# Optimization experiments

Measured on AMD Instinct MI355X. Metric: run time of the kernel, lower is better.

Reference implementation:

```python
import jax, jax.numpy as jnp
import numpy as np

B, C, F, NH, DK, DV = 16, 256, 32, 8, 32, 64
S = F * F
EPS = 1e-5
SCALE = DK ** -0.5


def _bn(t, g, b, m, v):
    # t: [B, Ch, H, W]; eval-mode batchnorm with running stats
    inv = g / jnp.sqrt(v + EPS)
    return t * inv[None, :, None, None] + (b - m * inv)[None, :, None, None]


def setup_inputs() -> dict:
    key = jax.random.key(0)
    ks = jax.random.split(key, 24)
    n = lambda i, shape, s=0.05: jax.random.normal(ks[i], shape, jnp.float32) * s
    u = lambda i, shape: jax.random.uniform(ks[i], shape, jnp.float32, 0.5, 1.5)
    # relative-position index table (buffer)
    r = np.arange(F)
    pos = np.stack(np.meshgrid(r, r, indexing='ij'), axis=-1).reshape(-1, 2)
    rel = np.abs(pos[:, None, :] - pos[None, :, :])
    pos_indices = jnp.asarray(rel[..., 0] * F + rel[..., 1], jnp.int32)  # [S, S]
    return {
        'x': jax.random.normal(ks[0], (B, C, F, F), jnp.float32),
        'Wq': n(1, (NH * DK, C)), 'q_g': u(2, (NH * DK,)), 'q_b': n(3, (NH * DK,)), 'q_m': n(4, (NH * DK,)), 'q_v': u(5, (NH * DK,)),
        'Wk': n(6, (NH * DK, C)), 'k_g': u(7, (NH * DK,)), 'k_b': n(8, (NH * DK,)), 'k_m': n(9, (NH * DK,)), 'k_v': u(10, (NH * DK,)),
        'Wv': n(11, (NH * DV, C)), 'v_g': u(12, (NH * DV,)), 'v_b': n(13, (NH * DV,)), 'v_m': n(14, (NH * DV,)), 'v_v': u(15, (NH * DV,)),
        'pos_emb': n(16, (F * F, NH)),
        'Wo': n(17, (C, NH * DV)), 'bo': n(18, (C,)),
        'o_g': u(19, (C,)), 'o_b': n(20, (C,)), 'o_m': n(21, (C,)), 'o_v': u(22, (C,)),
        'pos_indices': pos_indices,
    }


def reference(x, Wq, q_g, q_b, q_m, q_v, Wk, k_g, k_b, k_m, k_v, Wv, v_g, v_b, v_m, v_v,
              pos_emb, Wo, bo, o_g, o_b, o_m, o_v, pos_indices):
    # 1x1 conv == channel GEMM
    q = _bn(jnp.einsum('bchw,oc->bohw', x, Wq), q_g, q_b, q_m, q_v)
    k = _bn(jnp.einsum('bchw,oc->bohw', x, Wk), k_g, k_b, k_m, k_v)
    v = _bn(jnp.einsum('bchw,oc->bohw', x, Wv), v_g, v_b, v_m, v_v)
    # b (n d) h w -> b n s d
    qh = q.reshape(B, NH, DK, S).transpose(0, 1, 3, 2)
    kh = k.reshape(B, NH, DK, S).transpose(0, 1, 3, 2)
    vh = v.reshape(B, NH, DV, S).transpose(0, 1, 3, 2)
    attn = jnp.einsum('bnqd,bnkd->bnqk', qh, kh) * SCALE  # [B, NH, S, S]
    bias = pos_emb[pos_indices]                            # [S, S, NH] gather
    attn = attn + jnp.transpose(bias, (2, 0, 1))[None] / SCALE
    attn = jax.nn.softmax(attn, axis=-1)
    o = jnp.einsum('bnqk,bnkd->bnqd', attn, vh)            # [B, NH, S, DV]
    o = o.transpose(0, 1, 3, 2).reshape(B, NH * DV, F, F)  # b (n d) h w
    o = jax.nn.gelu(o, approximate=False)                  # torch default GELU (erf)
    o = jnp.einsum('bchw,oc->bohw', o, Wo) + bo[None, :, None, None]
    return _bn(o, o_g, o_b, o_m, o_v)
```

## Files before the change

kernel.cpp:

```cpp
#include <hip/hip_runtime.h>

#define B_ 16
#define C_ 256
#define NH_ 8
#define DK_ 32
#define DV_ 64
#define S_ 1024
#define CV_ 512

typedef __bf16 bf16;
typedef bf16 bf16x4 __attribute__((ext_vector_type(4)));
typedef bf16 bf16x8 __attribute__((ext_vector_type(8)));
typedef float f32x4 __attribute__((ext_vector_type(4)));

constexpr float EPSV = 1e-5f;
constexpr float SCALE_ = 0.17677669529663687f;
constexpr float LOG2E_ = 1.4426950408889634f;
constexpr float QSCALE_ = SCALE_ * LOG2E_;
constexpr float BSCALE_ = (1.0f / SCALE_) * LOG2E_;

__global__ void prep_kernel(const float* __restrict__ Wq, const float* __restrict__ qg, const float* __restrict__ qb, const float* __restrict__ qm, const float* __restrict__ qv,
                            const float* __restrict__ Wk, const float* __restrict__ kg, const float* __restrict__ kb, const float* __restrict__ km, const float* __restrict__ kv,
                            const float* __restrict__ Wv, const float* __restrict__ vg, const float* __restrict__ vb, const float* __restrict__ vm, const float* __restrict__ vv,
                            const float* __restrict__ Wo, const float* __restrict__ bo, const float* __restrict__ og_, const float* __restrict__ ob_, const float* __restrict__ om_, const float* __restrict__ ov_,
                            bf16* __restrict__ wqkv, float* __restrict__ bqkv, bf16* __restrict__ wo2, float* __restrict__ bo2) {
  int idx = blockIdx.x * 256 + threadIdx.x;
  if (idx < 1024 * 256) {
    int o = idx >> 8, c = idx & 255;
    float w, g, v;
    if (o < 256)      { w = Wq[o * 256 + c];        g = qg[o];       v = qv[o]; }
    else if (o < 512) { w = Wk[(o - 256) * 256 + c]; g = kg[o - 256]; v = kv[o - 256]; }
    else              { w = Wv[(o - 512) * 256 + c]; g = vg[o - 512]; v = vv[o - 512]; }
    float inv = g * rsqrtf(v + EPSV);
    wqkv[idx] = (bf16)(w * inv);
    if (c == 0) {
      float bb, m;
      if (o < 256)      { bb = qb[o];       m = qm[o]; }
      else if (o < 512) { bb = kb[o - 256]; m = km[o - 256]; }
      else              { bb = vb[o - 512]; m = vm[o - 512]; }
      bqkv[o] = bb - m * inv;
    }
  } else {
    int j = idx - 1024 * 256;
    if (j < 256 * 512) {
      int co = j >> 9, cv = j & 511;
      float inv = og_[co] * rsqrtf(ov_[co] + EPSV);
      wo2[j] = (bf16)(Wo[j] * inv);
      if (cv == 0) bo2[co] = bo[co] * inv + ob_[co] - om_[co] * inv;
    }
  }
}

__global__ __launch_bounds__(256) void xpose_kernel(const float* __restrict__ x, bf16* __restrict__ xT) {
  __shared__ bf16 t[64][66];
  int b = blockIdx.z, c0 = blockIdx.y * 64, s0 = blockIdx.x * 64;
  const float* xp = x + ((size_t)b * C_ + c0) * S_ + s0;
#pragma unroll
  for (int p = 0; p < 4; ++p) {
    int q = p * 256 + threadIdx.x;
    int ci = q >> 4, si4 = (q & 15) * 4;
    float4 v = *(const float4*)(xp + (size_t)ci * S_ + si4);
    t[si4 + 0][ci] = (bf16)v.x;
    t[si4 + 1][ci] = (bf16)v.y;
    t[si4 + 2][ci] = (bf16)v.z;
    t[si4 + 3][ci] = (bf16)v.w;
  }
  __syncthreads();
  bf16* op = xT + ((size_t)b * S_ + s0) * C_ + c0;
#pragma unroll
  for (int p = 0; p < 4; ++p) {
    int q = p * 256 + threadIdx.x;
    int si = q >> 4, ci4 = (q & 15) * 4;
    bf16x4 pk;
#pragma unroll
    for (int e = 0; e < 4; ++e) pk[e] = t[si][ci4 + e];
    *(bf16x4*)(op + (size_t)si * C_ + ci4) = pk;
  }
}

__device__ __forceinline__ void gload16(const void* g, void* l) {
  __builtin_amdgcn_global_load_lds((const __attribute__((address_space(1))) void*)g,
                                   (__attribute__((address_space(3))) void*)l, 16, 0, 0);
}

__global__ __launch_bounds__(256) void qkv_gemm_kernel(const bf16* __restrict__ wqkv, const float* __restrict__ bqkv,
                                                       const bf16* __restrict__ xT, bf16* __restrict__ qh,
                                                       bf16* __restrict__ kh, bf16* __restrict__ vT) {
  __shared__ bf16 alds[2][128 * 32];
  __shared__ bf16 blds[2][128 * 32];
  const int b = blockIdx.z;
  const int ob = blockIdx.y * 128, sb = blockIdx.x * 128;
  const int w = threadIdx.x >> 6, lane = threadIdx.x & 63;
  const int g = lane >> 4, lo = lane & 15;
  const int ow = (w >> 1) * 64, sw = (w & 1) * 64;

  const int r0 = threadIdx.x >> 2, c4 = threadIdx.x & 3;
  const int swz = (c4 ^ ((r0 >> 1) & 3)) * 8;
  const bf16* aS = wqkv + (size_t)(ob + r0) * C_ + swz;
  const bf16* bS = xT + ((size_t)b * S_ + sb + r0) * C_ + swz;
  const int ldst = threadIdx.x * 8;
  auto stage = [&](int buf, int kc) {
    gload16(aS + kc, &alds[buf][ldst]);
    gload16(aS + (size_t)64 * C_ + kc, &alds[buf][ldst + 2048]);
    gload16(bS + kc, &blds[buf][ldst]);
    gload16(bS + (size_t)64 * C_ + kc, &blds[buf][ldst + 2048]);
  };

  f32x4 acc[4][4] = {};

  stage(0, 0);
  __syncthreads();

  for (int step = 0; step < 8; ++step) {
    const int cur = step & 1;
    if (step < 7) stage(cur ^ 1, (step + 1) * 32);
    bf16x8 af[4], bfr[4];
    const int ch = (g ^ ((lo >> 1) & 3)) * 8;
#pragma unroll
    for (int i = 0; i < 4; ++i)
      af[i] = *(const bf16x8*)(&alds[cur][(ow + i * 16 + lo) * 32 + ch]);
#pragma unroll
    for (int j = 0; j < 4; ++j)
      bfr[j] = *(const bf16x8*)(&blds[cur][(sw + j * 16 + lo) * 32 + ch]);
#pragma unroll
    for (int i = 0; i < 4; ++i)
#pragma unroll
      for (int j = 0; j < 4; ++j)
        acc[i][j] = __builtin_amdgcn_mfma_f32_16x16x32_bf16(af[i], bfr[j], acc[i][j], 0, 0, 0);
    __syncthreads();
  }

#pragma unroll
  for (int i = 0; i < 4; ++i) {
    const int o0 = ob + ow + i * 16 + 4 * g;
    const bool isv = o0 >= 512;
    const bool isq = o0 < 256;
    float bias4[4];
#pragma unroll
    for (int r = 0; r < 4; ++r) bias4[r] = bqkv[o0 + r];
#pragma unroll
    for (int j = 0; j < 4; ++j) {
      const int s = sb + sw + j * 16 + lo;
      if (!isv) {
        const int n = (o0 >> 5) & 7;
        const int d0 = o0 & 31;
        bf16x4 pk;
#pragma unroll
        for (int r = 0; r < 4; ++r) {
          float v = acc[i][j][r] + bias4[r];
          pk[r] = (bf16)(isq ? v * QSCALE_ : v);
        }
        bf16* dst = (isq ? qh : kh) + (((size_t)b * NH_ + n) * S_ + s) * DK_ + d0;
        *(bf16x4*)dst = pk;
      } else {
        const int o2 = o0 - 512;
        const int n = o2 >> 6, dv0 = o2 & 63;
#pragma unroll
        for (int r = 0; r < 4; ++r)
          vT[(((size_t)b * NH_ + n) * DV_ + dv0 + r) * S_ + s] = (bf16)(acc[i][j][r] + bias4[r]);
      }
    }
  }
}

__global__ __launch_bounds__(512, 4) void attn_kernel(const bf16* __restrict__ qh, const bf16* __restrict__ kh,
                                                      const bf16* __restrict__ vT, const float* __restrict__ pos_emb,
                                                      bf16* __restrict__ og) {
  __shared__ f32x4 E4[32][64];
  __shared__ bf16 klds[2][64 * 32];
  __shared__ bf16 vlds[2][64 * 64];
  const int n = blockIdx.x, qt = blockIdx.y, b = blockIdx.z;
  const int w = threadIdx.x >> 6, lane = threadIdx.x & 63;
  const int g = lane >> 4, lo = lane & 15;
  const size_t bn = (size_t)b * NH_ + n;
  const bf16* __restrict__ kbase = kh + bn * (size_t)S_ * DK_;
  const bf16* __restrict__ vbase = vT + bn * (size_t)DV_ * S_;

  const int krow = (w & 3) * 16 + (lane >> 2), kslot = lane & 3;
  const int vrow = w * 8 + (lane >> 3), vslot = lane & 7;
  const bf16* ksrc0 = kbase + (size_t)krow * DK_ + ((kslot ^ ((krow >> 2) & 3)) * 8);
  const bf16* vsrc0 = vbase + (size_t)vrow * S_ + ((vslot ^ (vrow & 7)) * 8);
  auto stage = [&](int buf, int kt) {
    if (w < 4) gload16(ksrc0 + (size_t)kt * DK_, &klds[buf][(w & 3) * 512]);
    gload16(vsrc0 + kt, &vlds[buf][w * 512]);
  };

  stage(0, 0);

  for (int i = threadIdx.x; i < 32 * 64; i += 512) {
    const int dr = i >> 6, d = i & 63;
    f32x4 v;
#pragma unroll
    for (int j = 0; j < 4; ++j) {
      int dc = d - 28 - j;
      dc = dc < 0 ? -dc : dc;
      dc = dc > 31 ? 31 : dc;
      v[j] = pos_emb[(dr * 32 + dc) * NH_ + n] * BSCALE_;
    }
    E4[dr][d] = v;
  }

  const int qbase = qt * 256 + w * 32;
  const int q0 = qbase + lo, q1 = qbase + 16 + lo;
  const bf16x8 qf0 = *(const bf16x8*)(qh + (bn * S_ + q0) * DK_ + 8 * g);
  const bf16x8 qf1 = *(const bf16x8*)(qh + (bn * S_ + q1) * DK_ + 8 * g);
  const int qr = qbase >> 5;
  const int i00m = 12 + lo - 4 * g;

  f32x4 acc[4][2] = {};
  f32x4 lac[2] = {};
  bf16x8 ones;
#pragma unroll
  for (int j = 0; j < 8; ++j) ones[j] = (bf16)1.0f;

  asm volatile("s_waitcnt vmcnt(0)" ::: "memory");
  __syncthreads();

  const f32x4* __restrict__ E4f = &E4[0][0];

  for (int it = 0; it < 16; ++it) {
    const int kt = it * 64;
    const int cur = it & 1;
    if (it < 15) stage(cur ^ 1, kt + 64);
    const bf16* kbuf = &klds[cur][0];
    const bf16* vbuf = &vlds[cur][0];

    int dq = qr - 2 * it;
    int dra = dq < 0 ? -dq : dq;
    int dqb = dq - 1;
    int drb = dqb < 0 ? -dqb : dqb;
    const f32x4* pa = E4f + dra * 64 + i00m;
    const f32x4* pbq = E4f + drb * 64 + i00m;
    const f32x4 W0a = pa[16], W0b = pbq[16];

    bf16x8 pb[2][2];
#pragma unroll
    for (int u = 0; u < 4; ++u) {
      const int row = u * 16 + lo;
      bf16x8 ka = *(const bf16x8*)(kbuf + row * 32 + ((8 * g) ^ (((row >> 2) & 3) << 3)));
      f32x4 c0, c1;
      if (u == 0)      { c0 = W0a;    c1 = pa[32]; }
      else if (u == 1) { c0 = pa[0];  c1 = W0a; }
      else if (u == 2) { c0 = W0b;    c1 = pbq[32]; }
      else             { c0 = pbq[0]; c1 = W0b; }
      f32x4 s0 = __builtin_amdgcn_mfma_f32_16x16x32_bf16(ka, qf0, c0, 0, 0, 0);
      f32x4 s1 = __builtin_amdgcn_mfma_f32_16x16x32_bf16(ka, qf1, c1, 0, 0, 0);
      const int cb = (u & 1) * 4;
      const int up = u >> 1;
#pragma unroll
      for (int r = 0; r < 4; ++r) {
        pb[0][up][cb + r] = (bf16)__builtin_amdgcn_exp2f(s0[r]);
        pb[1][up][cb + r] = (bf16)__builtin_amdgcn_exp2f(s1[r]);
      }
    }

    __builtin_amdgcn_s_setprio(1);
    lac[0] = __builtin_amdgcn_mfma_f32_16x16x32_bf16(ones, pb[0][0], lac[0], 0, 0, 0);
    lac[0] = __builtin_amdgcn_mfma_f32_16x16x32_bf16(ones, pb[0][1], lac[0], 0, 0, 0);
    lac[1] = __builtin_amdgcn_mfma_f32_16x16x32_bf16(ones, pb[1][0], lac[1], 0, 0, 0);
    lac[1] = __builtin_amdgcn_mfma_f32_16x16x32_bf16(ones, pb[1][1], lac[1], 0, 0, 0);

#pragma unroll
    for (int t = 0; t < 4; ++t) {
      const int row = t * 16 + lo;
      const int rsw = row & 7;
      const bf16* vrow_p = vbuf + row * 64 + 4 * (g & 1);
      const int ghalf = g >> 1;
#pragma unroll
      for (int up = 0; up < 2; ++up) {
        bf16x4 a0 = *(const bf16x4*)(vrow_p + ((((4 * up + 0) + ghalf) ^ rsw) << 3));
        bf16x4 a1 = *(const bf16x4*)(vrow_p + ((((4 * up + 2) + ghalf) ^ rsw) << 3));
        bf16x8 va = __builtin_shufflevector(a0, a1, 0, 1, 2, 3, 4, 5, 6, 7);
        acc[t][0] = __builtin_amdgcn_mfma_f32_16x16x32_bf16(va, pb[0][up], acc[t][0], 0, 0, 0);
        acc[t][1] = __builtin_amdgcn_mfma_f32_16x16x32_bf16(va, pb[1][up], acc[t][1], 0, 0, 0);
      }
    }
    __builtin_amdgcn_s_setprio(0);

    asm volatile("s_waitcnt vmcnt(0)" ::: "memory");
    __syncthreads();
  }

#pragma unroll
  for (int h = 0; h < 2; ++h) {
    const float rinv = __builtin_amdgcn_rcpf(lac[h][0]);
    const int qx = qbase + 16 * h + lo;
    bf16* op = og + ((size_t)b * S_ + qx) * CV_ + n * DV_;
#pragma unroll
    for (int t = 0; t < 4; ++t) {
      bf16x4 pk;
#pragma unroll
      for (int r = 0; r < 4; ++r) {
        float xo = acc[t][h][r] * rinv;
        pk[r] = (bf16)(0.5f * xo * (1.f + erff(xo * 0.70710678118654752f)));
      }
      *(bf16x4*)(op + t * 16 + 4 * g) = pk;
    }
  }
}

__global__ __launch_bounds__(256) void out_gemm_kernel(const bf16* __restrict__ wo2, const float* __restrict__ bo2,
                                                       const bf16* __restrict__ og, float* __restrict__ out) {
  __shared__ bf16 alds[2][64 * 32];
  __shared__ bf16 blds[2][128 * 32];
  const int b = blockIdx.z;
  const int cb = blockIdx.y * 64, sb = blockIdx.x * 128;
  const int w = threadIdx.x >> 6, lane = threadIdx.x & 63;
  const int g = lane >> 4, lo = lane & 15;
  const int cw = (w >> 1) * 32, sw = (w & 1) * 64;

  const int r0 = threadIdx.x >> 2, c4 = threadIdx.x & 3;
  const int swz = (c4 ^ ((r0 >> 1) & 3)) * 8;
  const bf16* aS = wo2 + (size_t)(cb + r0) * CV_ + swz;
  const bf16* bS = og + ((size_t)b * S_ + sb + r0) * CV_ + swz;
  const int ldst = threadIdx.x * 8;
  auto stage = [&](int buf, int kc) {
    gload16(aS + kc, &alds[buf][ldst]);
    gload16(bS + kc, &blds[buf][ldst]);
    gload16(bS + (size_t)64 * CV_ + kc, &blds[buf][ldst + 2048]);
  };

  f32x4 acc[2][4] = {};

  stage(0, 0);
  __syncthreads();

  for (int step = 0; step < 16; ++step) {
    const int cur = step & 1;
    if (step < 15) stage(cur ^ 1, (step + 1) * 32);
    bf16x8 af[2], bfr[4];
    const int ch = (g ^ ((lo >> 1) & 3)) * 8;
#pragma unroll
    for (int i = 0; i < 2; ++i)
      af[i] = *(const bf16x8*)(&alds[cur][(cw + i * 16 + lo) * 32 + ch]);
#pragma unroll
    for (int j = 0; j < 4; ++j)
      bfr[j] = *(const bf16x8*)(&blds[cur][(sw + j * 16 + lo) * 32 + ch]);
#pragma unroll
    for (int i = 0; i < 2; ++i)
#pragma unroll
      for (int j = 0; j < 4; ++j)
        acc[i][j] = __builtin_amdgcn_mfma_f32_16x16x32_bf16(af[i], bfr[j], acc[i][j], 0, 0, 0);
    __syncthreads();
  }

#pragma unroll
  for (int i = 0; i < 2; ++i) {
    const int c0 = cb + cw + i * 16 + 4 * g;
    float bias4[4];
#pragma unroll
    for (int r = 0; r < 4; ++r) bias4[r] = bo2[c0 + r];
#pragma unroll
    for (int j = 0; j < 4; ++j) {
      const int s = sb + sw + j * 16 + lo;
#pragma unroll
      for (int r = 0; r < 4; ++r)
        out[((size_t)b * C_ + c0 + r) * S_ + s] = acc[i][j][r] + bias4[r];
    }
  }
}

extern "C" void kernel_launch(void* const* d_in, const int* in_sizes, int n_in,
                              void* d_out, int out_size, void* d_ws, size_t ws_size,
                              hipStream_t stream) {
  (void)in_sizes; (void)n_in; (void)out_size; (void)ws_size;
  const float* x   = (const float*)d_in[0];
  const float* Wq  = (const float*)d_in[1];
  const float* qg  = (const float*)d_in[2];
  const float* qb  = (const float*)d_in[3];
  const float* qm  = (const float*)d_in[4];
  const float* qv  = (const float*)d_in[5];
  const float* Wk  = (const float*)d_in[6];
  const float* kg  = (const float*)d_in[7];
  const float* kb  = (const float*)d_in[8];
  const float* km  = (const float*)d_in[9];
  const float* kv  = (const float*)d_in[10];
  const float* Wv  = (const float*)d_in[11];
  const float* vg  = (const float*)d_in[12];
  const float* vb  = (const float*)d_in[13];
  const float* vm  = (const float*)d_in[14];
  const float* vv  = (const float*)d_in[15];
  const float* pos = (const float*)d_in[16];
  const float* Wo  = (const float*)d_in[17];
  const float* bo  = (const float*)d_in[18];
  const float* ogm = (const float*)d_in[19];
  const float* obt = (const float*)d_in[20];
  const float* omn = (const float*)d_in[21];
  const float* ovr = (const float*)d_in[22];
  float* out = (float*)d_out;

  char* ws = (char*)d_ws;
  size_t off = 0;
  auto take = [&](size_t bytes) { char* p = ws + off; off += (bytes + 255) & ~(size_t)255; return p; };
  bf16*  wqkv = (bf16*) take((size_t)1024 * 256 * 2);
  float* bqkv = (float*)take(1024 * 4);
  bf16*  wo2  = (bf16*) take((size_t)256 * 512 * 2);
  float* bo2  = (float*)take(256 * 4);
  bf16*  xT   = (bf16*) take((size_t)B_ * S_ * C_ * 2);
  bf16*  qhb  = (bf16*) take((size_t)B_ * NH_ * S_ * DK_ * 2);
  bf16*  khb  = (bf16*) take((size_t)B_ * NH_ * S_ * DK_ * 2);
  bf16*  vTb  = (bf16*) take((size_t)B_ * NH_ * DV_ * S_ * 2);
  bf16*  ogb  = (bf16*) take((size_t)B_ * S_ * CV_ * 2);

  prep_kernel<<<dim3(1536), dim3(256), 0, stream>>>(Wq, qg, qb, qm, qv, Wk, kg, kb, km, kv,
                                                    Wv, vg, vb, vm, vv, Wo, bo, ogm, obt, omn, ovr,
                                                    wqkv, bqkv, wo2, bo2);
  xpose_kernel<<<dim3(16, 4, 16), dim3(256), 0, stream>>>(x, xT);
  qkv_gemm_kernel<<<dim3(8, 8, 16), dim3(256), 0, stream>>>(wqkv, bqkv, xT, qhb, khb, vTb);
  attn_kernel<<<dim3(8, 4, 16), dim3(512), 0, stream>>>(qhb, khb, vTb, pos, ogb);
  out_gemm_kernel<<<dim3(8, 4, 16), dim3(256), 0, stream>>>(wo2, bo2, ogb, out);
}
```

Baseline: 90.38 us.

## Split attention key range across two wave groups with LDS reduction, bf16 bias table

Each attention block now covers 128 queries instead of 256, and its two halves of 4 waves each process separate halves of the key sequence in 32-key tiles. Partial outputs and row sums are combined through LDS before the GELU epilogue. The block count doubles and launch bounds are raised, aiming at more parallelism and occupancy. The position-bias table is stored in bf16 to cut LDS use, which loses some precision in the bias and in the bf16-rounded partial outputs.

```diff
diff --git a/kernel.cpp b/kernel.cpp
--- a/kernel.cpp
+++ b/kernel.cpp
@@ -163,49 +163,53 @@
   }
 }
 
-__global__ __launch_bounds__(512, 4) void attn_kernel(const bf16* __restrict__ qh, const bf16* __restrict__ kh,
+__global__ __launch_bounds__(512, 8) void attn_kernel(const bf16* __restrict__ qh, const bf16* __restrict__ kh,
                                                       const bf16* __restrict__ vT, const float* __restrict__ pos_emb,
                                                       bf16* __restrict__ og) {
-  __shared__ f32x4 E4[32][64];
-  __shared__ bf16 klds[2][64 * 32];
-  __shared__ bf16 vlds[2][64 * 64];
+  __shared__ __align__(16) char smem[40960];
+  bf16* E4b = (bf16*)smem;
+  bf16* kld = (bf16*)(smem + 16384);
+  bf16* vld = (bf16*)(smem + 24576);
   const int n = blockIdx.x, qt = blockIdx.y, b = blockIdx.z;
   const int w = threadIdx.x >> 6, lane = threadIdx.x & 63;
   const int g = lane >> 4, lo = lane & 15;
+  const int h2 = w >> 2, wg = w & 3;
   const size_t bn = (size_t)b * NH_ + n;
   const bf16* __restrict__ kbase = kh + bn * (size_t)S_ * DK_;
   const bf16* __restrict__ vbase = vT + bn * (size_t)DV_ * S_;
-
-  const int krow = (w & 3) * 16 + (lane >> 2), kslot = lane & 3;
-  const int vrow = w * 8 + (lane >> 3), vslot = lane & 7;
-  const bf16* ksrc0 = kbase + (size_t)krow * DK_ + ((kslot ^ ((krow >> 2) & 3)) * 8);
-  const bf16* vsrc0 = vbase + (size_t)vrow * S_ + ((vslot ^ (vrow & 7)) * 8);
+  const int kt0 = h2 * 512;
+
+  const int krow = wg * 16 + (lane >> 2), kcs = lane & 3;
+  const bf16* ksrc0 = kbase + (size_t)(kt0 + krow) * DK_ + ((kcs ^ ((krow >> 1) & 3)) * 8);
+  const bf16* vsrc0 = vbase + (size_t)krow * S_ + kt0 + ((kcs ^ ((krow >> 1) & 3)) * 8);
+  bf16* kH = kld + h2 * 2048;
+  bf16* vH = vld + h2 * 4096;
   auto stage = [&](int buf, int kt) {
-    if (w < 4) gload16(ksrc0 + (size_t)kt * DK_, &klds[buf][(w & 3) * 512]);
-    gload16(vsrc0 + kt, &vlds[buf][w * 512]);
+    if (wg < 2) gload16(ksrc0 + (size_t)kt * DK_, kH + buf * 1024 + wg * 512);
+    gload16(vsrc0 + kt, vH + buf * 2048 + wg * 512);
   };
 
   stage(0, 0);
 
-  for (int i = threadIdx.x; i < 32 * 64; i += 512) {
+  for (int i = threadIdx.x; i < 2048; i += 512) {
     const int dr = i >> 6, d = i & 63;
-    f32x4 v;
+    bf16x4 v;
 #pragma unroll
     for (int j = 0; j < 4; ++j) {
       int dc = d - 28 - j;
       dc = dc < 0 ? -dc : dc;
       dc = dc > 31 ? 31 : dc;
-      v[j] = pos_emb[(dr * 32 + dc) * NH_ + n] * BSCALE_;
-    }
-    E4[dr][d] = v;
-  }
-
-  const int qbase = qt * 256 + w * 32;
+      v[j] = (bf16)(pos_emb[(dr * 32 + dc) * NH_ + n] * BSCALE_);
+    }
+    *(bf16x4*)(E4b + (size_t)i * 4) = v;
+  }
+
+  const int qbase = qt * 128 + wg * 32;
   const int q0 = qbase + lo, q1 = qbase + 16 + lo;
   const bf16x8 qf0 = *(const bf16x8*)(qh + (bn * S_ + q0) * DK_ + 8 * g);
   const bf16x8 qf1 = *(const bf16x8*)(qh + (bn * S_ + q1) * DK_ + 8 * g);
   const int qr = qbase >> 5;
-  const int i00m = 12 + lo - 4 * g;
+  const bf16* Qb = E4b + (12 + lo - 4 * g) * 4;
 
   f32x4 acc[4][2] = {};
   f32x4 lac[2] = {};
@@ -213,67 +217,53 @@
 #pragma unroll
   for (int j = 0; j < 8; ++j) ones[j] = (bf16)1.0f;
 
-  asm volatile("s_waitcnt vmcnt(0)" ::: "memory");
   __syncthreads();
 
-  const f32x4* __restrict__ E4f = &E4[0][0];
-
   for (int it = 0; it < 16; ++it) {
-    const int kt = it * 64;
+    const int kt = it * 32;
     const int cur = it & 1;
-    if (it < 15) stage(cur ^ 1, kt + 64);
-    const bf16* kbuf = &klds[cur][0];
-    const bf16* vbuf = &vlds[cur][0];
-
-    int dq = qr - 2 * it;
+    if (it < 15) stage(cur ^ 1, kt + 32);
+    const bf16* kbuf = kH + cur * 1024;
+    const bf16* vbuf = vH + cur * 2048;
+
+    int dq = qr - (h2 * 16 + it);
     int dra = dq < 0 ? -dq : dq;
-    int dqb = dq - 1;
-    int drb = dqb < 0 ? -dqb : dqb;
-    const f32x4* pa = E4f + dra * 64 + i00m;
-    const f32x4* pbq = E4f + drb * 64 + i00m;
-    const f32x4 W0a = pa[16], W0b = pbq[16];
-
-    bf16x8 pb[2][2];
-#pragma unroll
-    for (int u = 0; u < 4; ++u) {
+    const bf16* Qr = Qb + dra * 256;
+    bf16x4 b0q = *(const bf16x4*)(Qr);
+    bf16x4 b16 = *(const bf16x4*)(Qr + 64);
+    bf16x4 b32 = *(const bf16x4*)(Qr + 128);
+    f32x4 C0, C16, C32;
+#pragma unroll
+    for (int e = 0; e < 4; ++e) { C0[e] = (float)b0q[e]; C16[e] = (float)b16[e]; C32[e] = (float)b32[e]; }
+
+    bf16x8 pb[2];
+#pragma unroll
+    for (int u = 0; u < 2; ++u) {
       const int row = u * 16 + lo;
-      bf16x8 ka = *(const bf16x8*)(kbuf + row * 32 + ((8 * g) ^ (((row >> 2) & 3) << 3)));
-      f32x4 c0, c1;
-      if (u == 0)      { c0 = W0a;    c1 = pa[32]; }
-      else if (u == 1) { c0 = pa[0];  c1 = W0a; }
-      else if (u == 2) { c0 = W0b;    c1 = pbq[32]; }
-      else             { c0 = pbq[0]; c1 = W0b; }
-      f32x4 s0 = __builtin_amdgcn_mfma_f32_16x16x32_bf16(ka, qf0, c0, 0, 0, 0);
-      f32x4 s1 = __builtin_amdgcn_mfma_f32_16x16x32_bf16(ka, qf1, c1, 0, 0, 0);
-      const int cb = (u & 1) * 4;
-      const int up = u >> 1;
+      bf16x8 ka = *(const bf16x8*)(kbuf + row * 32 + ((g ^ ((row >> 1) & 3)) * 8));
+      f32x4 s0 = __builtin_amdgcn_mfma_f32_16x16x32_bf16(ka, qf0, u == 0 ? C16 : C0, 0, 0, 0);
+      f32x4 s1 = __builtin_amdgcn_mfma_f32_16x16x32_bf16(ka, qf1, u == 0 ? C32 : C16, 0, 0, 0);
 #pragma unroll
       for (int r = 0; r < 4; ++r) {
-        pb[0][up][cb + r] = (bf16)__builtin_amdgcn_exp2f(s0[r]);
-        pb[1][up][cb + r] = (bf16)__builtin_amdgcn_exp2f(s1[r]);
+        pb[0][u * 4 + r] = (bf16)__builtin_amdgcn_exp2f(s0[r]);
+        pb[1][u * 4 + r] = (bf16)__builtin_amdgcn_exp2f(s1[r]);
       }
     }
 
     __builtin_amdgcn_s_setprio(1);
-    lac[0] = __builtin_amdgcn_mfma_f32_16x16x32_bf16(ones, pb[0][0], lac[0], 0, 0, 0);
-    lac[0] = __builtin_amdgcn_mfma_f32_16x16x32_bf16(ones, pb[0][1], lac[0], 0, 0, 0);
-    lac[1] = __builtin_amdgcn_mfma_f32_16x16x32_bf16(ones, pb[1][0], lac[1], 0, 0, 0);
-    lac[1] = __builtin_amdgcn_mfma_f32_16x16x32_bf16(ones, pb[1][1], lac[1], 0, 0, 0);
+    lac[0] = __builtin_amdgcn_mfma_f32_16x16x32_bf16(ones, pb[0], lac[0], 0, 0, 0);
+    lac[1] = __builtin_amdgcn_mfma_f32_16x16x32_bf16(ones, pb[1], lac[1], 0, 0, 0);
 
 #pragma unroll
     for (int t = 0; t < 4; ++t) {
       const int row = t * 16 + lo;
-      const int rsw = row & 7;
-      const bf16* vrow_p = vbuf + row * 64 + 4 * (g & 1);
-      const int ghalf = g >> 1;
-#pragma unroll
-      for (int up = 0; up < 2; ++up) {
-        bf16x4 a0 = *(const bf16x4*)(vrow_p + ((((4 * up + 0) + ghalf) ^ rsw) << 3));
-        bf16x4 a1 = *(const bf16x4*)(vrow_p + ((((4 * up + 2) + ghalf) ^ rsw) << 3));
-        bf16x8 va = __builtin_shufflevector(a0, a1, 0, 1, 2, 3, 4, 5, 6, 7);
-        acc[t][0] = __builtin_amdgcn_mfma_f32_16x16x32_bf16(va, pb[0][up], acc[t][0], 0, 0, 0);
-        acc[t][1] = __builtin_amdgcn_mfma_f32_16x16x32_bf16(va, pb[1][up], acc[t][1], 0, 0, 0);
-      }
+      const int rs = (row >> 1) & 3;
+      const bf16* vr = vbuf + row * 32 + ((g & 1) << 2);
+      bf16x4 p0 = *(const bf16x4*)(vr + ((((g >> 1) + 0) ^ rs) << 3));
+      bf16x4 p1 = *(const bf16x4*)(vr + ((((g >> 1) + 2) ^ rs) << 3));
+      bf16x8 va = __builtin_shufflevector(p0, p1, 0, 1, 2, 3, 4, 5, 6, 7);
+      acc[t][0] = __builtin_amdgcn_mfma_f32_16x16x32_bf16(va, pb[0], acc[t][0], 0, 0, 0);
+      acc[t][1] = __builtin_amdgcn_mfma_f32_16x16x32_bf16(va, pb[1], acc[t][1], 0, 0, 0);
     }
     __builtin_amdgcn_s_setprio(0);
 
@@ -281,20 +271,39 @@
     __syncthreads();
   }
 
-#pragma unroll
-  for (int h = 0; h < 2; ++h) {
-    const float rinv = __builtin_amdgcn_rcpf(lac[h][0]);
-    const int qx = qbase + 16 * h + lo;
-    bf16* op = og + ((size_t)b * S_ + qx) * CV_ + n * DV_;
-#pragma unroll
-    for (int t = 0; t < 4; ++t) {
-      bf16x4 pk;
-#pragma unroll
-      for (int r = 0; r < 4; ++r) {
-        float xo = acc[t][h][r] * rinv;
-        pk[r] = (bf16)(0.5f * xo * (1.f + erff(xo * 0.70710678118654752f)));
+  bf16* Sc = (bf16*)smem;
+  float* Sl = (float*)(smem + 16384);
+  if (h2) {
+#pragma unroll
+    for (int t = 0; t < 4; ++t)
+#pragma unroll
+      for (int h = 0; h < 2; ++h) {
+        bf16x4 pk;
+#pragma unroll
+        for (int r = 0; r < 4; ++r) pk[r] = (bf16)acc[t][h][r];
+        *(bf16x4*)(Sc + (size_t)(wg * 32 + 16 * h + lo) * 64 + 16 * t + 4 * g) = pk;
       }
-      *(bf16x4*)(op + t * 16 + 4 * g) = pk;
+    if (g == 0) { Sl[wg * 32 + lo] = lac[0][0]; Sl[wg * 32 + 16 + lo] = lac[1][0]; }
+  }
+  __syncthreads();
+  if (!h2) {
+#pragma unroll
+    for (int h = 0; h < 2; ++h) {
+      const float lB = Sl[wg * 32 + 16 * h + lo];
+      const float rinv = __builtin_amdgcn_rcpf(lac[h][0] + lB);
+      const int qx = qbase + 16 * h + lo;
+      bf16* op = og + ((size_t)b * S_ + qx) * CV_ + n * DV_;
+#pragma unroll
+      for (int t = 0; t < 4; ++t) {
+        bf16x4 pB = *(const bf16x4*)(Sc + (size_t)(wg * 32 + 16 * h + lo) * 64 + 16 * t + 4 * g);
+        bf16x4 pk;
+#pragma unroll
+        for (int r = 0; r < 4; ++r) {
+          float xo = (acc[t][h][r] + (float)pB[r]) * rinv;
+          pk[r] = (bf16)(0.5f * xo * (1.f + erff(xo * 0.70710678118654752f)));
+        }
+        *(bf16x4*)(op + t * 16 + 4 * g) = pk;
+      }
     }
   }
 }
@@ -407,6 +416,6 @@
                                                     wqkv, bqkv, wo2, bo2);
   xpose_kernel<<<dim3(16, 4, 16), dim3(256), 0, stream>>>(x, xT);
   qkv_gemm_kernel<<<dim3(8, 8, 16), dim3(256), 0, stream>>>(wqkv, bqkv, xT, qhb, khb, vTb);
-  attn_kernel<<<dim3(8, 4, 16), dim3(512), 0, stream>>>(qhb, khb, vTb, pos, ogb);
+  attn_kernel<<<dim3(8, 8, 16), dim3(512), 0, stream>>>(qhb, khb, vTb, pos, ogb);
   out_gemm_kernel<<<dim3(8, 4, 16), dim3(256), 0, stream>>>(wo2, bo2, ogb, out);
 }
```

After: 282.9 us. 3.13x slower.

## Double key-tile depth per barrier and store position bias table in bf16

Applied to the files above, without the earlier changes.

Each pipeline stage now loads two 64-key tiles of K and V, halving the number of loop iterations and __syncthreads barriers. The bias table moves from f32 to bf16 so the larger staging buffers fit in shared memory. All eight waves now share the K loading. The cost is roughly double the LDS footprint for K/V, which may reduce occupancy, plus bf16 rounding of the positional bias.

```diff
diff --git a/kernel.cpp b/kernel.cpp
--- a/kernel.cpp
+++ b/kernel.cpp
@@ -166,9 +166,9 @@
 __global__ __launch_bounds__(512, 4) void attn_kernel(const bf16* __restrict__ qh, const bf16* __restrict__ kh,
                                                       const bf16* __restrict__ vT, const float* __restrict__ pos_emb,
                                                       bf16* __restrict__ og) {
-  __shared__ f32x4 E4[32][64];
-  __shared__ bf16 klds[2][64 * 32];
-  __shared__ bf16 vlds[2][64 * 64];
+  __shared__ __align__(16) bf16 E4b[32 * 64 * 4];
+  __shared__ bf16 klds[2 * 2 * 64 * 32];
+  __shared__ bf16 vlds[2 * 2 * 64 * 64];
   const int n = blockIdx.x, qt = blockIdx.y, b = blockIdx.z;
   const int w = threadIdx.x >> 6, lane = threadIdx.x & 63;
   const int g = lane >> 4, lo = lane & 15;
@@ -180,24 +180,26 @@
   const int vrow = w * 8 + (lane >> 3), vslot = lane & 7;
   const bf16* ksrc0 = kbase + (size_t)krow * DK_ + ((kslot ^ ((krow >> 2) & 3)) * 8);
   const bf16* vsrc0 = vbase + (size_t)vrow * S_ + ((vslot ^ (vrow & 7)) * 8);
+  const int ksub = w >> 2;
   auto stage = [&](int buf, int kt) {
-    if (w < 4) gload16(ksrc0 + (size_t)kt * DK_, &klds[buf][(w & 3) * 512]);
-    gload16(vsrc0 + kt, &vlds[buf][w * 512]);
+    gload16(ksrc0 + (size_t)(kt + ksub * 64) * DK_, &klds[(buf * 2 + ksub) * 2048 + (w & 3) * 512]);
+    gload16(vsrc0 + kt,      &vlds[(buf * 2 + 0) * 4096 + w * 512]);
+    gload16(vsrc0 + kt + 64, &vlds[(buf * 2 + 1) * 4096 + w * 512]);
   };
 
   stage(0, 0);
 
-  for (int i = threadIdx.x; i < 32 * 64; i += 512) {
+  for (int i = threadIdx.x; i < 2048; i += 512) {
     const int dr = i >> 6, d = i & 63;
-    f32x4 v;
+    bf16x4 v;
 #pragma unroll
     for (int j = 0; j < 4; ++j) {
       int dc = d - 28 - j;
       dc = dc < 0 ? -dc : dc;
       dc = dc > 31 ? 31 : dc;
-      v[j] = pos_emb[(dr * 32 + dc) * NH_ + n] * BSCALE_;
-    }
-    E4[dr][d] = v;
+      v[j] = (bf16)(pos_emb[(dr * 32 + dc) * NH_ + n] * BSCALE_);
+    }
+    *(bf16x4*)(E4b + (size_t)i * 4) = v;
   }
 
   const int qbase = qt * 256 + w * 32;
@@ -205,7 +207,7 @@
   const bf16x8 qf0 = *(const bf16x8*)(qh + (bn * S_ + q0) * DK_ + 8 * g);
   const bf16x8 qf1 = *(const bf16x8*)(qh + (bn * S_ + q1) * DK_ + 8 * g);
   const int qr = qbase >> 5;
-  const int i00m = 12 + lo - 4 * g;
+  const bf16* Qb = E4b + (12 + lo - 4 * g) * 4;
 
   f32x4 acc[4][2] = {};
   f32x4 lac[2] = {};
@@ -216,66 +218,76 @@
   asm volatile("s_waitcnt vmcnt(0)" ::: "memory");
   __syncthreads();
 
-  const f32x4* __restrict__ E4f = &E4[0][0];
-
-  for (int it = 0; it < 16; ++it) {
-    const int kt = it * 64;
+  for (int it = 0; it < 8; ++it) {
+    const int kt = it * 128;
     const int cur = it & 1;
-    if (it < 15) stage(cur ^ 1, kt + 64);
-    const bf16* kbuf = &klds[cur][0];
-    const bf16* vbuf = &vlds[cur][0];
-
-    int dq = qr - 2 * it;
-    int dra = dq < 0 ? -dq : dq;
-    int dqb = dq - 1;
-    int drb = dqb < 0 ? -dqb : dqb;
-    const f32x4* pa = E4f + dra * 64 + i00m;
-    const f32x4* pbq = E4f + drb * 64 + i00m;
-    const f32x4 W0a = pa[16], W0b = pbq[16];
-
-    bf16x8 pb[2][2];
-#pragma unroll
-    for (int u = 0; u < 4; ++u) {
-      const int row = u * 16 + lo;
-      bf16x8 ka = *(const bf16x8*)(kbuf + row * 32 + ((8 * g) ^ (((row >> 2) & 3) << 3)));
-      f32x4 c0, c1;
-      if (u == 0)      { c0 = W0a;    c1 = pa[32]; }
-      else if (u == 1) { c0 = pa[0];  c1 = W0a; }
-      else if (u == 2) { c0 = W0b;    c1 = pbq[32]; }
-      else             { c0 = pbq[0]; c1 = W0b; }
-      f32x4 s0 = __builtin_amdgcn_mfma_f32_16x16x32_bf16(ka, qf0, c0, 0, 0, 0);
-      f32x4 s1 = __builtin_amdgcn_mfma_f32_16x16x32_bf16(ka, qf1, c1, 0, 0, 0);
-      const int cb = (u & 1) * 4;
-      const int up = u >> 1;
-#pragma unroll
-      for (int r = 0; r < 4; ++r) {
-        pb[0][up][cb + r] = (bf16)__builtin_amdgcn_exp2f(s0[r]);
-        pb[1][up][cb + r] = (bf16)__builtin_amdgcn_exp2f(s1[r]);
+    if (it < 7) stage(cur ^ 1, kt + 128);
+
+#pragma unroll
+    for (int sub = 0; sub < 2; ++sub) {
+      const bf16* kbuf = &klds[(cur * 2 + sub) * 2048];
+      const bf16* vbuf = &vlds[(cur * 2 + sub) * 4096];
+      const int ts = 2 * it + sub;
+
+      int dq = qr - 2 * ts;
+      int dra = dq < 0 ? -dq : dq;
+      int dqb = dq - 1;
+      int drb = dqb < 0 ? -dqb : dqb;
+      const bf16* QA = Qb + dra * 256;
+      const bf16* QP = Qb + drb * 256;
+      bf16x4 qa0 = *(const bf16x4*)(QA), qa1 = *(const bf16x4*)(QA + 64), qa2 = *(const bf16x4*)(QA + 128);
+      bf16x4 qp0 = *(const bf16x4*)(QP), qp1 = *(const bf16x4*)(QP + 64), qp2 = *(const bf16x4*)(QP + 128);
+      f32x4 a0, a16, a32, b0, b16, b32;
+#pragma unroll
+      for (int e = 0; e < 4; ++e) {
+        a0[e] = (float)qa0[e]; a16[e] = (float)qa1[e]; a32[e] = (float)qa2[e];
+        b0[e] = (float)qp0[e]; b16[e] = (float)qp1[e]; b32[e] = (float)qp2[e];
       }
-    }
-
-    __builtin_amdgcn_s_setprio(1);
-    lac[0] = __builtin_amdgcn_mfma_f32_16x16x32_bf16(ones, pb[0][0], lac[0], 0, 0, 0);
-    lac[0] = __builtin_amdgcn_mfma_f32_16x16x32_bf16(ones, pb[0][1], lac[0], 0, 0, 0);
-    lac[1] = __builtin_amdgcn_mfma_f32_16x16x32_bf16(ones, pb[1][0], lac[1], 0, 0, 0);
-    lac[1] = __builtin_amdgcn_mfma_f32_16x16x32_bf16(ones, pb[1][1], lac[1], 0, 0, 0);
-
-#pragma unroll
-    for (int t = 0; t < 4; ++t) {
-      const int row = t * 16 + lo;
-      const int rsw = row & 7;
-      const bf16* vrow_p = vbuf + row * 64 + 4 * (g & 1);
-      const int ghalf = g >> 1;
-#pragma unroll
-      for (int up = 0; up < 2; ++up) {
-        bf16x4 a0 = *(const bf16x4*)(vrow_p + ((((4 * up + 0) + ghalf) ^ rsw) << 3));
-        bf16x4 a1 = *(const bf16x4*)(vrow_p + ((((4 * up + 2) + ghalf) ^ rsw) << 3));
-        bf16x8 va = __builtin_shufflevector(a0, a1, 0, 1, 2, 3, 4, 5, 6, 7);
-        acc[t][0] = __builtin_amdgcn_mfma_f32_16x16x32_bf16(va, pb[0][up], acc[t][0], 0, 0, 0);
-        acc[t][1] = __builtin_amdgcn_mfma_f32_16x16x32_bf16(va, pb[1][up], acc[t][1], 0, 0, 0);
+
+      bf16x8 pb[2][2];
+#pragma unroll
+      for (int u = 0; u < 4; ++u) {
+        const int row = u * 16 + lo;
+        bf16x8 ka = *(const bf16x8*)(kbuf + row * 32 + ((8 * g) ^ (((row >> 2) & 3) << 3)));
+        f32x4 c0, c1;
+        if (u == 0)      { c0 = a16; c1 = a32; }
+        else if (u == 1) { c0 = a0;  c1 = a16; }
+        else if (u == 2) { c0 = b16; c1 = b32; }
+        else             { c0 = b0;  c1 = b16; }
+        f32x4 s0 = __builtin_amdgcn_mfma_f32_16x16x32_bf16(ka, qf0, c0, 0, 0, 0);
+        f32x4 s1 = __builtin_amdgcn_mfma_f32_16x16x32_bf16(ka, qf1, c1, 0, 0, 0);
+        const int cb = (u & 1) * 4;
+        const int up = u >> 1;
+#pragma unroll
+        for (int r = 0; r < 4; ++r) {
+          pb[0][up][cb + r] = (bf16)__builtin_amdgcn_exp2f(s0[r]);
+          pb[1][up][cb + r] = (bf16)__builtin_amdgcn_exp2f(s1[r]);
+        }
       }
-    }
-    __builtin_amdgcn_s_setprio(0);
+
+      __builtin_amdgcn_s_setprio(1);
+      lac[0] = __builtin_amdgcn_mfma_f32_16x16x32_bf16(ones, pb[0][0], lac[0], 0, 0, 0);
+      lac[0] = __builtin_amdgcn_mfma_f32_16x16x32_bf16(ones, pb[0][1], lac[0], 0, 0, 0);
+      lac[1] = __builtin_amdgcn_mfma_f32_16x16x32_bf16(ones, pb[1][0], lac[1], 0, 0, 0);
+      lac[1] = __builtin_amdgcn_mfma_f32_16x16x32_bf16(ones, pb[1][1], lac[1], 0, 0, 0);
+
+#pragma unroll
+      for (int t = 0; t < 4; ++t) {
+        const int row = t * 16 + lo;
+        const int rsw = row & 7;
+        const bf16* vrow_p = vbuf + row * 64 + 4 * (g & 1);
+        const int ghalf = g >> 1;
+#pragma unroll
+        for (int up = 0; up < 2; ++up) {
+          bf16x4 va0 = *(const bf16x4*)(vrow_p + ((((4 * up + 0) + ghalf) ^ rsw) << 3));
+          bf16x4 va1 = *(const bf16x4*)(vrow_p + ((((4 * up + 2) + ghalf) ^ rsw) << 3));
+          bf16x8 va = __builtin_shufflevector(va0, va1, 0, 1, 2, 3, 4, 5, 6, 7);
+          acc[t][0] = __builtin_amdgcn_mfma_f32_16x16x32_bf16(va, pb[0][up], acc[t][0], 0, 0, 0);
+          acc[t][1] = __builtin_amdgcn_mfma_f32_16x16x32_bf16(va, pb[1][up], acc[t][1], 0, 0, 0);
+        }
+      }
+      __builtin_amdgcn_s_setprio(0);
+    }
 
     asm volatile("s_waitcnt vmcnt(0)" ::: "memory");
     __syncthreads();
```

Result: no change. 90.90 us (+0.6%).
